# Kernel tuning notes

Hardware: AMD Instinct MI355X
Metric: run time of the kernel (lower is better)

The kernel has to match this reference:

```python
import jax, jax.numpy as jnp
import numpy as np

K = 8          # num groups / object slots
FC = 256       # fc_size
LAST = 128     # last_fc_size
B = 2048       # batch
M = 1024       # input size
H = 512        # state (hidden) size


def _ln(x, g, b):
    # LayerNorm over last dim, eps matches torch default 1e-5
    mu = jnp.mean(x, axis=-1, keepdims=True)
    var = jnp.mean((x - mu) ** 2, axis=-1, keepdims=True)
    return (x - mu) * jax.lax.rsqrt(var + 1e-5) * g + b


def setup_inputs() -> dict:
    key = jax.random.key(0)
    ks = jax.random.split(key, 10)
    s = 0.05
    d = {
        "x": jax.random.normal(ks[0], (B * K, M), jnp.float32),
        "state": jax.random.normal(ks[1], (B * K, H), jnp.float32),
        # encoder: Linear(H->FC) + LN(FC)
        "enc_w": jax.random.normal(ks[2], (H, FC), jnp.float32) * s,
        "enc_b": jnp.zeros((FC,), jnp.float32),
        "enc_g": jnp.ones((FC,), jnp.float32),
        "enc_bb": jnp.zeros((FC,), jnp.float32),
        # core: Linear(2*FC->FC) + LN(FC)
        "core_w": jax.random.normal(ks[3], (2 * FC, FC), jnp.float32) * s,
        "core_b": jnp.zeros((FC,), jnp.float32),
        "core_g": jnp.ones((FC,), jnp.float32),
        "core_bb": jnp.zeros((FC,), jnp.float32),
        # context: Linear(FC->FC) + LN(FC)
        "ctx_w": jax.random.normal(ks[4], (FC, FC), jnp.float32) * s,
        "ctx_b": jnp.zeros((FC,), jnp.float32),
        "ctx_g": jnp.ones((FC,), jnp.float32),
        "ctx_bb": jnp.zeros((FC,), jnp.float32),
        # attention: Linear(FC->LAST) + LN(LAST) + Tanh + Linear(LAST->1) + Sigmoid
        "att1_w": jax.random.normal(ks[5], (FC, LAST), jnp.float32) * s,
        "att1_b": jnp.zeros((LAST,), jnp.float32),
        "att_g": jnp.ones((LAST,), jnp.float32),
        "att_bb": jnp.zeros((LAST,), jnp.float32),
        "att2_w": jax.random.normal(ks[6], (LAST, 1), jnp.float32) * s,
        "att2_b": jnp.zeros((1,), jnp.float32),
        # out_fc: Linear(FC + FC + M -> FC)
        "out_w": jax.random.normal(ks[7], (FC + FC + M, FC), jnp.float32) * s,
        "out_b": jnp.zeros((FC,), jnp.float32),
    }
    return d


def reference(x, state, enc_w, enc_b, enc_g, enc_bb,
              core_w, core_b, core_g, core_bb,
              ctx_w, ctx_b, ctx_g, ctx_bb,
              att1_w, att1_b, att_g, att_bb, att2_w, att2_b,
              out_w, out_b):
    bk, m = x.shape
    k = K
    b = bk // k
    # 0. encode state: [B*K, H] -> [B*K, FC]
    s1 = jax.nn.relu(_ln(state @ enc_w + enc_b, enc_g, enc_bb))
    h1 = s1.shape[-1]
    s1r = s1.reshape(b, k, h1)
    # focus: K-1 copies of each slot's state  [b, k, k-1, h1]
    fs = jnp.broadcast_to(s1r[:, :, None, :], (b, k, k - 1, h1))
    # context: gather the K-1 other slots' states (replaces torch python loop)
    idx = np.array([[j for j in range(k) if j != i] for i in range(k)])  # [k, k-1]
    cs = s1r[:, idx, :]  # [b, k, k-1, h1]
    concat = jnp.concatenate([fs, cs], axis=-1).reshape(b * k * (k - 1), 2 * h1)
    # core / context MLPs over pairs
    core = jax.nn.relu(_ln(concat @ core_w + core_b, core_g, core_bb))   # [b*k*(k-1), FC]
    ctx = jax.nn.relu(_ln(core @ ctx_w + ctx_b, ctx_g, ctx_bb))          # [b*k*(k-1), FC]
    # attention scalar per pair
    att_h = jnp.tanh(_ln(core @ att1_w + att1_b, att_g, att_bb))
    att = jax.nn.sigmoid(att_h @ att2_w + att2_b)                        # [b*k*(k-1), 1]
    # attention-weighted sum over the K-1 context dim
    h2 = ctx.shape[-1]
    effect = jnp.sum(ctx.reshape(b * k, k - 1, h2) * att.reshape(b * k, k - 1, 1), axis=1)
    # decode: concat encoded state, effect, input -> new state
    total = jnp.concatenate([s1, effect, x], axis=-1)
    new_state = total @ out_w + out_b
    return (new_state, new_state)
```

## Files before the change

kernel.cpp:

```cpp
#include <hip/hip_runtime.h>
#include <stdint.h>

#define FC    256
#define HH    512
#define MX    1024
#define LASTN 128
#define NROW  16384
#define NGRP  2048

typedef unsigned short u16;
typedef __bf16 bf16x8 __attribute__((ext_vector_type(8)));
typedef float  f32x4  __attribute__((ext_vector_type(4)));

__device__ __forceinline__ float red16(float v) {
#pragma unroll
  for (int m = 1; m < 16; m <<= 1) v += __shfl_xor(v, m);
  return v;
}
__device__ __forceinline__ float red16hi(float v) {
#pragma unroll
  for (int m = 4; m < 64; m <<= 1) v += __shfl_xor(v, m);
  return v;
}
__device__ __forceinline__ u16 to_bf16(float f) {
  unsigned u = __float_as_uint(f);
  return (u16)((u + 0x8000u) >> 16);
}
__device__ __forceinline__ float from_bf16(u16 s) {
  return __uint_as_float(((unsigned)s) << 16);
}
__device__ __forceinline__ uint32_t pk2(float a, float b) {
  return (uint32_t)to_bf16(a) | ((uint32_t)to_bf16(b) << 16);
}
__device__ __forceinline__ float tanh_fast(float x) {
  float e = __expf(2.f * x);
  return __fdividef(e - 1.f, e + 1.f);
}
__device__ __forceinline__ float sigmoid_fast(float x) {
  return __fdividef(1.f, 1.f + __expf(-x));
}
__device__ __forceinline__ void glds16(const void* g, void* l) {
  __builtin_amdgcn_global_load_lds(
      (__attribute__((address_space(1))) uint32_t*)g,
      (__attribute__((address_space(3))) uint32_t*)l, 16, 0, 0);
}
__device__ __forceinline__ bf16x8 frag_ld(const u16* p) {
  return __builtin_bit_cast(bf16x8, *(const uint4*)p);
}

__global__ __launch_bounds__(256) void k_prep(
    const float* __restrict__ enc_w, const float* __restrict__ core_w,
    const float* __restrict__ ctx_w, const float* __restrict__ att1_w,
    const float* __restrict__ out_w,
    u16* __restrict__ encT, u16* __restrict__ uvT, u16* __restrict__ ctxT,
    u16* __restrict__ attT, u16* __restrict__ outT)
{
  const int bx = blockIdx.x, tid = threadIdx.x;
  const float* W; u16* D; int NKC, N, local; int uv = 0;
  if (bx < 64)       { W = enc_w;  D = encT; NKC = 16; N = 256; local = bx * 256 + tid; }
  else if (bx < 128) { W = core_w; D = uvT;  NKC = 8;  N = 256; local = (bx-64)*256 + tid; uv = 1; }
  else if (bx < 160) { W = ctx_w;  D = ctxT; NKC = 8;  N = 256; local = (bx-128)*256 + tid; }
  else if (bx < 176) { W = att1_w; D = attT; NKC = 8;  N = 128; local = (bx-160)*256 + tid; }
  else               { W = out_w;  D = outT; NKC = 48; N = 256; local = (bx-176)*256 + tid; }
  const int l  = local & 63;
  const int kc = (local >> 6) % NKC;
  const int u  = (local >> 6) / NKC;
  const int n  = u * 16 + (l & 15);
  const int k0 = kc * 32 + (l >> 4) * 8;
  float f[8];
#pragma unroll
  for (int j = 0; j < 8; ++j) {
    const int k = k0 + j;
    if (uv) f[j] = (n < 256) ? W[(size_t)k * 256 + n] : W[(size_t)(256 + k) * 256 + (n - 256)];
    else    f[j] = W[(size_t)k * N + n];
  }
  uint4 w;
  w.x = pk2(f[0], f[1]); w.y = pk2(f[2], f[3]);
  w.z = pk2(f[4], f[5]); w.w = pk2(f[6], f[7]);
  *(uint4*)&D[(size_t)local * 8] = w;
}

__global__ __launch_bounds__(256) void k_enc(
    const float* __restrict__ state, const u16* __restrict__ encT,
    const float* __restrict__ enc_b, const float* __restrict__ enc_g,
    const float* __restrict__ enc_bb, u16* __restrict__ s1b)
{
  __shared__ __align__(16) u16 smA[2][128 * 8];
  __shared__ __align__(16) u16 smB[2][16 * 64 * 8];
  __shared__ float smP[2][2][16][2];
  const int tid = threadIdx.x, wv = tid >> 6, lane = tid & 63;
  const int cl = lane & 15, quad = lane >> 4;
  const int rb = wv >> 1, cb = wv & 1;
  const int row0 = blockIdx.x * 32;
  f32x4 acc[8];
#pragma unroll
  for (int u = 0; u < 8; ++u) acc[u] = (f32x4){0.f, 0.f, 0.f, 0.f};

  for (int kk = 0; kk < 8; ++kk) {
    __syncthreads();
    {
      const int p = tid >> 7, lu = tid & 127;
      const int kc = kk * 2 + p;
      const int rblk = lu >> 6, ll = lu & 63;
      const float* src = state + (size_t)(row0 + rblk * 16 + (ll & 15)) * HH + kc * 32 + (ll >> 4) * 8;
      float4 a = *(const float4*)src, b = *(const float4*)(src + 4);
      uint4 w; w.x = pk2(a.x, a.y); w.y = pk2(a.z, a.w); w.z = pk2(b.x, b.y); w.w = pk2(b.z, b.w);
      *(uint4*)&smA[p][(size_t)lu * 8] = w;
    }
#pragma unroll
    for (int p = 0; p < 2; ++p)
#pragma unroll
      for (int i = 0; i < 4; ++i) {
        const int u = wv * 4 + i;
        glds16(encT + ((size_t)(u * 16 + kk * 2 + p) * 64 + lane) * 8, &smB[p][u * 512]);
      }
    __syncthreads();
#pragma unroll
    for (int p = 0; p < 2; ++p) {
      bf16x8 af = frag_ld(&smA[p][(rb * 64 + lane) * 8]);
#pragma unroll
      for (int u = 0; u < 8; ++u) {
        bf16x8 bf = frag_ld(&smB[p][((cb * 8 + u) * 64 + lane) * 8]);
        acc[u] = __builtin_amdgcn_mfma_f32_16x16x32_bf16(af, bf, acc[u], 0, 0, 0);
      }
    }
  }
  float bias[8], gg[8], bb[8];
#pragma unroll
  for (int u = 0; u < 8; ++u) {
    const int col = cb * 128 + u * 16 + cl;
    bias[u] = enc_b[col]; gg[u] = enc_g[col]; bb[u] = enc_bb[col];
  }
  float vv[4][8];
#pragma unroll
  for (int r4 = 0; r4 < 4; ++r4) {
    float s = 0.f, sq = 0.f;
#pragma unroll
    for (int u = 0; u < 8; ++u) {
      float v = acc[u][r4] + bias[u];
      vv[r4][u] = v; s += v; sq += v * v;
    }
    s = red16(s); sq = red16(sq);
    if (cl == 0) { smP[cb][rb][quad * 4 + r4][0] = s; smP[cb][rb][quad * 4 + r4][1] = sq; }
  }
  __syncthreads();
#pragma unroll
  for (int r4 = 0; r4 < 4; ++r4) {
    const int rr = quad * 4 + r4;
    const float S  = smP[0][rb][rr][0] + smP[1][rb][rr][0];
    const float SQ = smP[0][rb][rr][1] + smP[1][rb][rr][1];
    const float mu = S * (1.f / 256.f);
    const float rs = rsqrtf(SQ * (1.f / 256.f) - mu * mu + 1e-5f);
    const int row = row0 + rb * 16 + rr;
#pragma unroll
    for (int u = 0; u < 8; ++u) {
      float o = fmaxf((vv[r4][u] - mu) * rs * gg[u] + bb[u], 0.f);
      s1b[(size_t)row * FC + cb * 128 + u * 16 + cl] = to_bf16(o);
    }
  }
}

__global__ __launch_bounds__(256) void k_uv(
    const u16* __restrict__ s1b, const u16* __restrict__ uvT,
    float* __restrict__ UV)
{
  __shared__ __align__(16) u16 smA[2][4 * 64 * 8];
  __shared__ __align__(16) u16 smB[2][8 * 64 * 8];
  const int tid = threadIdx.x, wv = tid >> 6, lane = tid & 63;
  const int cl = lane & 15, quad = lane >> 4;
  const int row0 = blockIdx.x * 64;
  const int nb = blockIdx.y;
  f32x4 acc[8];
#pragma unroll
  for (int u = 0; u < 8; ++u) acc[u] = (f32x4){0.f, 0.f, 0.f, 0.f};

  for (int kk = 0; kk < 4; ++kk) {
    __syncthreads();
#pragma unroll
    for (int p = 0; p < 2; ++p) {
      const int kc = kk * 2 + p;
      glds16(s1b + (size_t)(row0 + wv * 16 + (lane & 15)) * FC + kc * 32 + (lane >> 4) * 8,
             &smA[p][wv * 512]);
#pragma unroll
      for (int i = 0; i < 2; ++i) {
        const int u = wv * 2 + i;
        glds16(uvT + ((size_t)((nb * 8 + u) * 8 + kc) * 64 + lane) * 8, &smB[p][u * 512]);
      }
    }
    __syncthreads();
#pragma unroll
    for (int p = 0; p < 2; ++p) {
      bf16x8 af = frag_ld(&smA[p][(wv * 64 + lane) * 8]);
#pragma unroll
      for (int u = 0; u < 8; ++u) {
        bf16x8 bf = frag_ld(&smB[p][(u * 64 + lane) * 8]);
        acc[u] = __builtin_amdgcn_mfma_f32_16x16x32_bf16(af, bf, acc[u], 0, 0, 0);
      }
    }
  }
#pragma unroll
  for (int r4 = 0; r4 < 4; ++r4) {
    const int row = row0 + wv * 16 + quad * 4 + r4;
#pragma unroll
    for (int u = 0; u < 8; ++u)
      UV[(size_t)row * 512 + nb * 128 + u * 16 + cl] = acc[u][r4];
  }
}

__global__ __launch_bounds__(256, 3) void k_pair(
    const float* __restrict__ UV, const float* __restrict__ core_b,
    const float* __restrict__ core_g, const float* __restrict__ core_bb,
    const u16* __restrict__ ctxT, const float* __restrict__ ctx_b,
    const float* __restrict__ ctx_g, const float* __restrict__ ctx_bb,
    const u16* __restrict__ attT, const float* __restrict__ att1_b,
    const float* __restrict__ att_g, const float* __restrict__ att_bb,
    const float* __restrict__ att2_w, const float* __restrict__ att2_b,
    u16* __restrict__ effb)
{
  __shared__ __align__(16) u16 smA[2048 * 8];
  __shared__ __align__(16) u16 smX[16 * 64 * 8];
  __shared__ float att_s[64];
  float* smUV = (float*)smX;
  u16*   smB  = smX;
  const int g = blockIdx.x;
  const int tid = threadIdx.x, wv = tid >> 6, lane = tid & 63;
  const int cl = lane & 15, quad = lane >> 4;
  const int aswz = ((lane >> 5) & 1) << 2;

#pragma unroll
  for (int i = 0; i < 4; ++i) {
    const int r = wv * 4 + i;
    const int row = g * 8 + (r & 7);
    const int half = r >> 3;
    glds16(UV + (size_t)row * 512 + half * 256 + lane * 4, &smUV[r * 256]);
  }
#pragma unroll
  for (int i = 0; i < 8; ++i)
    *(uint4*)&smA[(size_t)(tid + i * 256) * 8] = (uint4){0u, 0u, 0u, 0u};
  __syncthreads();

  {
    const int s4  = lane & 3;
    const int g16 = lane >> 2;
    const int c0  = g16 * 16;
    float4 CB[4], CG[4], CBB[4];
#pragma unroll
    for (int q = 0; q < 4; ++q) {
      const int cq = c0 + ((q ^ s4) << 2);
      CB[q]  = *(const float4*)&core_b[cq];
      CG[q]  = *(const float4*)&core_g[cq];
      CBB[q] = *(const float4*)&core_bb[cq];
    }
#pragma unroll
    for (int it = 0; it < 4; ++it) {
      const int p = it * 16 + wv * 4 + s4;
      if (p < 56) {
        const int i = p / 7, t = p - i * 7;
        const int j = t + (t >= i ? 1 : 0);
        const float* uA = &smUV[i * 256 + c0];
        const float* vB = &smUV[(8 + j) * 256 + c0];
        float v[16];
        float s = 0.f, sq = 0.f;
#pragma unroll
        for (int q = 0; q < 4; ++q) {
          const int qo = (q ^ s4) << 2;
          float4 ua = *(const float4*)(uA + qo);
          float4 vb = *(const float4*)(vB + qo);
          float x0 = ua.x + vb.x + CB[q].x, x1 = ua.y + vb.y + CB[q].y;
          float x2 = ua.z + vb.z + CB[q].z, x3 = ua.w + vb.w + CB[q].w;
          v[q*4+0] = x0; v[q*4+1] = x1; v[q*4+2] = x2; v[q*4+3] = x3;
          s += x0 + x1 + x2 + x3;
          sq += x0*x0 + x1*x1 + x2*x2 + x3*x3;
        }
        s = red16hi(s); sq = red16hi(sq);
        const float mu = s * (1.f / 256.f);
        const float rs = rsqrtf(sq * (1.f / 256.f) - mu * mu + 1e-5f);
#pragma unroll
        for (int q = 0; q < 4; ++q) {
          v[q*4+0] = fmaxf((v[q*4+0] - mu) * rs * CG[q].x + CBB[q].x, 0.f);
          v[q*4+1] = fmaxf((v[q*4+1] - mu) * rs * CG[q].y + CBB[q].y, 0.f);
          v[q*4+2] = fmaxf((v[q*4+2] - mu) * rs * CG[q].z + CBB[q].z, 0.f);
          v[q*4+3] = fmaxf((v[q*4+3] - mu) * rs * CG[q].w + CBB[q].w, 0.f);
        }
#pragma unroll
        for (int q = 0; q < 4; ++q) {
          const int lg = q ^ s4;
          const int ks = (g16 * 2 + (lg >> 1)) & 3;
          int slot = ((p >> 4) * 8 + (g16 >> 1)) * 64 + (p & 15) + 16 * ks;
          slot ^= ((slot >> 5) & 1) << 2;
          uint2 w;
          w.x = pk2(v[q*4+0], v[q*4+1]);
          w.y = pk2(v[q*4+2], v[q*4+3]);
          *(uint2*)&smA[(size_t)slot * 8 + (lg & 1) * 4] = w;
        }
      }
    }
  }
  __syncthreads();

  f32x4 accT[8];
#pragma unroll
  for (int t = 0; t < 8; ++t) accT[t] = (f32x4){0.f, 0.f, 0.f, 0.f};
#pragma unroll 2
  for (int kc = 0; kc < 8; ++kc) {
    uint4 attf[8];
#pragma unroll
    for (int q = 0; q < 8; ++q)
      attf[q] = *(const uint4*)(attT + ((size_t)(q * 8 + kc) * 64 + lane) * 8);
    bf16x8 af = frag_ld(&smA[(size_t)((((wv * 8 + kc) * 64) + lane) ^ aswz) * 8]);
#pragma unroll
    for (int q = 0; q < 8; ++q) {
      bf16x8 bf = __builtin_bit_cast(bf16x8, attf[q]);
      accT[q] = __builtin_amdgcn_mfma_f32_16x16x32_bf16(af, bf, accT[q], 0, 0, 0);
    }
  }

#pragma unroll
  for (int i = 0; i < 4; ++i) {
    const int q = wv * 4 + i;
    glds16(ctxT + ((size_t)(q * 8 + 0) * 64 + lane) * 8, &smB[q * 512]);
  }

  {
    float ab[8], ag[8], abb[8], aw[8];
#pragma unroll
    for (int t = 0; t < 8; ++t) {
      const int col = t * 16 + cl;
      ab[t] = att1_b[col]; ag[t] = att_g[col]; abb[t] = att_bb[col]; aw[t] = att2_w[col];
    }
    const float b2 = att2_b[0];
#pragma unroll
    for (int r4 = 0; r4 < 4; ++r4) {
      float v[8], s = 0.f, sq = 0.f;
#pragma unroll
      for (int t = 0; t < 8; ++t) {
        v[t] = accT[t][r4] + ab[t];
        s += v[t]; sq += v[t] * v[t];
      }
      s = red16(s); sq = red16(sq);
      const float mu = s * (1.f / 128.f);
      const float rs = rsqrtf(sq * (1.f / 128.f) - mu * mu + 1e-5f);
      float d = 0.f;
#pragma unroll
      for (int t = 0; t < 8; ++t) {
        float h = tanh_fast((v[t] - mu) * rs * ag[t] + abb[t]);
        d = fmaf(h, aw[t], d);
      }
      d = red16(d);
      if (cl == 0) {
        const int r = wv * 16 + quad * 4 + r4;
        if (r < 56) att_s[r] = sigmoid_fast(d + b2);
      }
    }
  }

  f32x4 accC[16];
#pragma unroll
  for (int t = 0; t < 16; ++t) accC[t] = (f32x4){0.f, 0.f, 0.f, 0.f};
  for (int kc = 0; kc < 8; ++kc) {
    __syncthreads();
    bf16x8 af = frag_ld(&smA[(size_t)((((wv * 8 + kc) * 64) + lane) ^ aswz) * 8]);
#pragma unroll
    for (int q = 0; q < 16; ++q) {
      bf16x8 bf = frag_ld(&smB[(q * 64 + lane) * 8]);
      accC[q] = __builtin_amdgcn_mfma_f32_16x16x32_bf16(af, bf, accC[q], 0, 0, 0);
    }
    __syncthreads();
    if (kc < 7) {
#pragma unroll
      for (int i = 0; i < 4; ++i) {
        const int q = wv * 4 + i;
        glds16(ctxT + ((size_t)(q * 8 + kc + 1) * 64 + lane) * 8, &smB[q * 512]);
      }
    }
  }

  u16* smS = smA;
  {
    float cb[16], cg[16], cbb[16];
#pragma unroll
    for (int t = 0; t < 16; ++t) {
      const int col = t * 16 + cl;
      cb[t] = ctx_b[col]; cg[t] = ctx_g[col]; cbb[t] = ctx_bb[col];
    }
#pragma unroll
    for (int r4 = 0; r4 < 4; ++r4) {
      float v[16], s = 0.f, sq = 0.f;
#pragma unroll
      for (int t = 0; t < 16; ++t) {
        v[t] = accC[t][r4] + cb[t];
        s += v[t]; sq += v[t] * v[t];
      }
      s = red16(s); sq = red16(sq);
      const float mu = s * (1.f / 256.f);
      const float rs = rsqrtf(sq * (1.f / 256.f) - mu * mu + 1e-5f);
      const int r = wv * 16 + quad * 4 + r4;
      if (r < 56) {
        const float ap = att_s[r];
#pragma unroll
        for (int t = 0; t < 16; ++t) {
          const int col = t * 16 + cl;
          float o = fmaxf((v[t] - mu) * rs * cg[t] + cbb[t], 0.f) * ap;
          smS[r * 264 + col] = to_bf16(o);
        }
      }
    }
  }
  __syncthreads();

  const int c = tid;
#pragma unroll
  for (int i = 0; i < 8; ++i) {
    float s = 0.f;
#pragma unroll
    for (int t2 = 0; t2 < 7; ++t2) s += from_bf16(smS[(i * 7 + t2) * 264 + c]);
    effb[(size_t)(g * 8 + i) * FC + c] = to_bf16(s);
  }
}

__global__ __launch_bounds__(256) void k_out(
    const u16* __restrict__ s1b, const u16* __restrict__ effb,
    const float* __restrict__ x, const u16* __restrict__ outT,
    const float* __restrict__ out_b, float* __restrict__ out, int dup)
{
  __shared__ __align__(16) u16 smA[2][2 * 64 * 8];
  __shared__ __align__(16) u16 smB[2][16 * 64 * 8];
  const int tid = threadIdx.x, wv = tid >> 6, lane = tid & 63;
  const int cl = lane & 15, quad = lane >> 4;
  const int row0 = blockIdx.x * 32;
  const int rw = wv >> 1;
  const int cw = wv & 1;
  f32x4 acc[8];
#pragma unroll
  for (int u = 0; u < 8; ++u) acc[u] = (f32x4){0.f, 0.f, 0.f, 0.f};

  for (int kk = 0; kk < 24; ++kk) {
    const int kc0 = kk * 2;
    __syncthreads();
    if (kc0 < 16) {
      const int p = wv >> 1, u = wv & 1;
      const int kc = kc0 + p;
      const u16* base = (kc < 8) ? s1b : effb;
      const int kof = (kc & 7) * 32;
      glds16(base + (size_t)(row0 + u * 16 + (lane & 15)) * FC + kof + (lane >> 4) * 8,
             &smA[p][u * 512]);
    } else {
      const int p = tid >> 7, lu = tid & 127;
      const int kc = kc0 + p;
      const int u = lu >> 6, l = lu & 63;
      const float* src = x + (size_t)(row0 + u * 16 + (l & 15)) * MX
                           + (kc - 16) * 32 + (l >> 4) * 8;
      float4 a = *(const float4*)src, b = *(const float4*)(src + 4);
      uint4 w; w.x = pk2(a.x, a.y); w.y = pk2(a.z, a.w); w.z = pk2(b.x, b.y); w.w = pk2(b.z, b.w);
      *(uint4*)&smA[p][(size_t)(u * 64 + l) * 8] = w;
    }
#pragma unroll
    for (int p = 0; p < 2; ++p)
#pragma unroll
      for (int i = 0; i < 4; ++i) {
        const int u = wv * 4 + i;
        glds16(outT + ((size_t)(u * 48 + kc0 + p) * 64 + lane) * 8, &smB[p][u * 512]);
      }
    __syncthreads();
#pragma unroll
    for (int p = 0; p < 2; ++p) {
      bf16x8 af = frag_ld(&smA[p][(rw * 64 + lane) * 8]);
#pragma unroll
      for (int i = 0; i < 8; ++i) {
        bf16x8 bf = frag_ld(&smB[p][((cw * 8 + i) * 64 + lane) * 8]);
        acc[i] = __builtin_amdgcn_mfma_f32_16x16x32_bf16(af, bf, acc[i], 0, 0, 0);
      }
    }
  }
  float bias[8];
#pragma unroll
  for (int i = 0; i < 8; ++i) bias[i] = out_b[cw * 128 + i * 16 + cl];
#pragma unroll
  for (int r4 = 0; r4 < 4; ++r4) {
    const int row = row0 + rw * 16 + quad * 4 + r4;
#pragma unroll
    for (int i = 0; i < 8; ++i) {
      const float o = acc[i][r4] + bias[i];
      const size_t off = (size_t)row * FC + cw * 128 + i * 16 + cl;
      out[off] = o;
      if (dup) out[(size_t)NROW * FC + off] = o;
    }
  }
}

extern "C" void kernel_launch(void* const* d_in, const int* in_sizes, int n_in,
                              void* d_out, int out_size, void* d_ws, size_t ws_size,
                              hipStream_t stream) {
  const float* x      = (const float*)d_in[0];
  const float* state  = (const float*)d_in[1];
  const float* enc_w  = (const float*)d_in[2];
  const float* enc_b  = (const float*)d_in[3];
  const float* enc_g  = (const float*)d_in[4];
  const float* enc_bb = (const float*)d_in[5];
  const float* core_w = (const float*)d_in[6];
  const float* core_b = (const float*)d_in[7];
  const float* core_g = (const float*)d_in[8];
  const float* core_bb= (const float*)d_in[9];
  const float* ctx_w  = (const float*)d_in[10];
  const float* ctx_b  = (const float*)d_in[11];
  const float* ctx_g  = (const float*)d_in[12];
  const float* ctx_bb = (const float*)d_in[13];
  const float* att1_w = (const float*)d_in[14];
  const float* att1_b = (const float*)d_in[15];
  const float* att_g  = (const float*)d_in[16];
  const float* att_bb = (const float*)d_in[17];
  const float* att2_w = (const float*)d_in[18];
  const float* att2_b = (const float*)d_in[19];
  const float* out_w  = (const float*)d_in[20];
  const float* out_b  = (const float*)d_in[21];

  char* ws = (char*)d_ws;
  float* UV  = (float*)ws;
  u16* s1b   = (u16*)(ws + 33554432);
  u16* effb  = (u16*)(ws + 41943040);
  u16* encT  = (u16*)(ws + 50331648);
  u16* uvT   = (u16*)(ws + 50593792);
  u16* ctxT  = (u16*)(ws + 50855936);
  u16* attT  = (u16*)(ws + 50987008);
  u16* outT  = (u16*)(ws + 51052544);
  float* out = (float*)d_out;
  const int dup = (out_size >= 2 * NROW * FC) ? 1 : 0;

  k_prep<<<dim3(368), 256, 0, stream>>>(enc_w, core_w, ctx_w, att1_w, out_w,
                                        encT, uvT, ctxT, attT, outT);
  k_enc<<<dim3(NROW / 32), 256, 0, stream>>>(state, encT, enc_b, enc_g, enc_bb, s1b);
  k_uv <<<dim3(NROW / 64, 4), 256, 0, stream>>>(s1b, uvT, UV);
  k_pair<<<dim3(NGRP), 256, 0, stream>>>(UV, core_b, core_g, core_bb,
                                         ctxT, ctx_b, ctx_g, ctx_bb,
                                         attT, att1_b, att_g, att_bb,
                                         att2_w, att2_b, effb);
  k_out<<<dim3(NROW / 32), 256, 0, stream>>>(s1b, effb, x, outT, out_b, out, dup);
}
```

Before: 285.7 us.

## Fuse UV projection GEMM into pair kernel, drop fp32 UV buffer

Removes the separate k_uv kernel that wrote a 32MB fp32 UV intermediate, and instead computes each group's 8-row UV projection inside k_pair with MFMA directly from s1b and uvT, writing results into shared memory. This eliminates the global round trip of the UV tensor and one launch. In exchange each block issues a 16-row MFMA tile where only 8 rows are useful, loads B fragments straight from global without LDS staging, and the extra register pressure may hurt occupancy under the 3-block launch bound.

```diff
diff --git a/kernel.cpp b/kernel.cpp
--- a/kernel.cpp
+++ b/kernel.cpp
@@ -160,55 +160,9 @@
   }
 }
 
-__global__ __launch_bounds__(256) void k_uv(
+__global__ __launch_bounds__(256, 3) void k_pair(
     const u16* __restrict__ s1b, const u16* __restrict__ uvT,
-    float* __restrict__ UV)
-{
-  __shared__ __align__(16) u16 smA[2][4 * 64 * 8];
-  __shared__ __align__(16) u16 smB[2][8 * 64 * 8];
-  const int tid = threadIdx.x, wv = tid >> 6, lane = tid & 63;
-  const int cl = lane & 15, quad = lane >> 4;
-  const int row0 = blockIdx.x * 64;
-  const int nb = blockIdx.y;
-  f32x4 acc[8];
-#pragma unroll
-  for (int u = 0; u < 8; ++u) acc[u] = (f32x4){0.f, 0.f, 0.f, 0.f};
-
-  for (int kk = 0; kk < 4; ++kk) {
-    __syncthreads();
-#pragma unroll
-    for (int p = 0; p < 2; ++p) {
-      const int kc = kk * 2 + p;
-      glds16(s1b + (size_t)(row0 + wv * 16 + (lane & 15)) * FC + kc * 32 + (lane >> 4) * 8,
-             &smA[p][wv * 512]);
-#pragma unroll
-      for (int i = 0; i < 2; ++i) {
-        const int u = wv * 2 + i;
-        glds16(uvT + ((size_t)((nb * 8 + u) * 8 + kc) * 64 + lane) * 8, &smB[p][u * 512]);
-      }
-    }
-    __syncthreads();
-#pragma unroll
-    for (int p = 0; p < 2; ++p) {
-      bf16x8 af = frag_ld(&smA[p][(wv * 64 + lane) * 8]);
-#pragma unroll
-      for (int u = 0; u < 8; ++u) {
-        bf16x8 bf = frag_ld(&smB[p][(u * 64 + lane) * 8]);
-        acc[u] = __builtin_amdgcn_mfma_f32_16x16x32_bf16(af, bf, acc[u], 0, 0, 0);
-      }
-    }
-  }
-#pragma unroll
-  for (int r4 = 0; r4 < 4; ++r4) {
-    const int row = row0 + wv * 16 + quad * 4 + r4;
-#pragma unroll
-    for (int u = 0; u < 8; ++u)
-      UV[(size_t)row * 512 + nb * 128 + u * 16 + cl] = acc[u][r4];
-  }
-}
-
-__global__ __launch_bounds__(256, 3) void k_pair(
-    const float* __restrict__ UV, const float* __restrict__ core_b,
+    const float* __restrict__ core_b,
     const float* __restrict__ core_g, const float* __restrict__ core_bb,
     const u16* __restrict__ ctxT, const float* __restrict__ ctx_b,
     const float* __restrict__ ctx_g, const float* __restrict__ ctx_bb,
@@ -228,15 +182,41 @@
   const int aswz = ((lane >> 5) & 1) << 2;
 
 #pragma unroll
-  for (int i = 0; i < 4; ++i) {
-    const int r = wv * 4 + i;
-    const int row = g * 8 + (r & 7);
-    const int half = r >> 3;
-    glds16(UV + (size_t)row * 512 + half * 256 + lane * 4, &smUV[r * 256]);
-  }
-#pragma unroll
   for (int i = 0; i < 8; ++i)
     *(uint4*)&smA[(size_t)(tid + i * 256) * 8] = (uint4){0u, 0u, 0u, 0u};
+
+  {
+    const int rowA = min(g * 8 + (lane & 15), NROW - 1);
+    const u16* aptr = s1b + (size_t)rowA * FC + (lane >> 4) * 8;
+    f32x4 accU[8];
+#pragma unroll
+    for (int u = 0; u < 8; ++u) accU[u] = (f32x4){0.f, 0.f, 0.f, 0.f};
+#pragma unroll 2
+    for (int kc = 0; kc < 8; ++kc) {
+      uint4 bfr[8];
+#pragma unroll
+      for (int u = 0; u < 8; ++u)
+        bfr[u] = *(const uint4*)(uvT + ((size_t)((wv * 8 + u) * 8 + kc) * 64 + lane) * 8);
+      bf16x8 af = frag_ld(aptr + kc * 32);
+#pragma unroll
+      for (int u = 0; u < 8; ++u) {
+        bf16x8 bf = __builtin_bit_cast(bf16x8, bfr[u]);
+        accU[u] = __builtin_amdgcn_mfma_f32_16x16x32_bf16(af, bf, accU[u], 0, 0, 0);
+      }
+    }
+#pragma unroll
+    for (int r4 = 0; r4 < 4; ++r4) {
+      const int r = quad * 4 + r4;
+      if (r < 8) {
+#pragma unroll
+        for (int u = 0; u < 8; ++u) {
+          const int c = wv * 128 + u * 16 + cl;
+          const int rr = (c >> 8) * 8 + r;
+          smUV[rr * 256 + (c & 255)] = accU[u][r4];
+        }
+      }
+    }
+  }
   __syncthreads();
 
   {
@@ -515,7 +495,6 @@
   const float* out_b  = (const float*)d_in[21];
 
   char* ws = (char*)d_ws;
-  float* UV  = (float*)ws;
   u16* s1b   = (u16*)(ws + 33554432);
   u16* effb  = (u16*)(ws + 41943040);
   u16* encT  = (u16*)(ws + 50331648);
@@ -529,8 +508,7 @@
   k_prep<<<dim3(368), 256, 0, stream>>>(enc_w, core_w, ctx_w, att1_w, out_w,
                                         encT, uvT, ctxT, attT, outT);
   k_enc<<<dim3(NROW / 32), 256, 0, stream>>>(state, encT, enc_b, enc_g, enc_bb, s1b);
-  k_uv <<<dim3(NROW / 64, 4), 256, 0, stream>>>(s1b, uvT, UV);
-  k_pair<<<dim3(NGRP), 256, 0, stream>>>(UV, core_b, core_g, core_bb,
+  k_pair<<<dim3(NGRP), 256, 0, stream>>>(s1b, uvT, core_b, core_g, core_bb,
                                          ctxT, ctx_b, ctx_g, ctx_bb,
                                          attT, att1_b, att_g, att_bb,
                                          att2_w, att2_b, effb);
```

After: 295.1 us. +3.3%, slower.
